# Kernel optimization log

Measured on AMD Instinct MI355X. Metric: run time of the kernel, lower is better.

The kernel has to match this reference:

```python
import jax, jax.numpy as jnp
import numpy as np

EMBED_DIM = 1024
FFN_DIM = 4096
N_QUBITS = 10


def setup_inputs() -> dict:
    key = jax.random.key(0)
    k_x, k_phi, k_w1, k_w2 = jax.random.split(key, 4)
    x = jax.random.normal(k_x, (8, 2048, EMBED_DIM), dtype=jnp.float32)
    # trainable RY angles, one per wire (torchquantum init ~ U(0, 2pi); any init works for a reference)
    ry_params = jax.random.uniform(k_phi, (N_QUBITS,), dtype=jnp.float32, minval=0.0, maxval=2.0 * np.pi)
    # nn.Linear(n_qubits, ffn_dim, bias=False): weight [ffn_dim, n_qubits]
    w1 = jax.random.normal(k_w1, (FFN_DIM, N_QUBITS), dtype=jnp.float32) / np.sqrt(N_QUBITS)
    # nn.Linear(ffn_dim, embed_dim, bias=False): weight [embed_dim, ffn_dim]
    w2 = jax.random.normal(k_w2, (EMBED_DIM, FFN_DIM), dtype=jnp.float32) / np.sqrt(FFN_DIM)
    return {"x": x, "ry_params": ry_params, "w1": w1, "w2": w2}


def reference(x, ry_params, w1, w2):
    # Quantum layer in closed form: wires are unentangled.
    # |0> --RX(x_i)--RY(phi_i)--> <Z_i> = cos(x_i) * cos(phi_i)
    # Only the first N_QUBITS features of each token are encoded.
    q_out = jnp.cos(x[..., :N_QUBITS]) * jnp.cos(ry_params)  # [B, S, nq]
    # dropout is identity in eval mode
    h = jnp.einsum('bsq,fq->bsf', q_out, w1)  # [B, S, ffn]
    h = jax.nn.relu(h)
    return jnp.einsum('bsf,ef->bse', h, w2)  # [B, S, embed]
```

## Files before the change

kernel.cpp:

```cpp
#include <hip/hip_runtime.h>
#include <stdint.h>

#define M_TOK   16384
#define EMBED   1024
#define FFN     4096
#define NQ      10

#define GK 4096
#define GN 1024
#define BK 64
#define NT (GK / BK)

typedef __attribute__((ext_vector_type(8))) short  bf16x8;
typedef __attribute__((ext_vector_type(4))) float  f32x4;
typedef __attribute__((ext_vector_type(8))) unsigned short u16x8;
typedef __attribute__((ext_vector_type(4))) unsigned short u16x4;

static __device__ __forceinline__ unsigned short f2bf(float f) {
    union { float f; unsigned u; } v; v.f = f;
    unsigned r = v.u + 0x7FFF + ((v.u >> 16) & 1);
    return (unsigned short)(r >> 16);
}

__global__ __launch_bounds__(256) void compute_h(
    const float* __restrict__ x, const float* __restrict__ ry,
    const float* __restrict__ w1, unsigned short* __restrict__ h)
{
    __shared__ float w1s[1024 * 11];
    __shared__ float cq[32 * 16];
    __shared__ float cry[16];

    const int tid = threadIdx.x;
    const int t0  = blockIdx.x * 32;
    const int f0  = blockIdx.y * 1024;

    if (tid < NQ) cry[tid] = cosf(ry[tid]);
    for (int idx = tid; idx < 32 * NQ; idx += 256) {
        int t = idx / NQ;
        int i = idx - t * NQ;
        cq[t * 16 + i] = cosf(x[(size_t)(t0 + t) * EMBED + i]);
    }
    for (int idx = tid; idx < (1024 * NQ) / 4; idx += 256) {
        float4 v = *(const float4*)(w1 + (size_t)f0 * NQ + idx * 4);
        int e = idx * 4;
#pragma unroll
        for (int k = 0; k < 4; ++k) {
            int ee = e + k;
            int r  = ee / NQ;
            int c  = ee - r * NQ;
            w1s[r * 11 + c] = ((const float*)&v)[k];
        }
    }
    __syncthreads();

    float wf[4][NQ];
#pragma unroll
    for (int fi = 0; fi < 4; ++fi)
#pragma unroll
        for (int i = 0; i < NQ; ++i)
            wf[fi][i] = w1s[(tid * 4 + fi) * 11 + i] * cry[i];

    for (int t = 0; t < 32; ++t) {
        const float4 c0 = *(const float4*)&cq[t * 16 + 0];
        const float4 c1 = *(const float4*)&cq[t * 16 + 4];
        const float2 c2 = *(const float2*)&cq[t * 16 + 8];
        u16x4 v;
#pragma unroll
        for (int fi = 0; fi < 4; ++fi) {
            float s = c0.x * wf[fi][0] + c0.y * wf[fi][1] + c0.z * wf[fi][2]
                    + c0.w * wf[fi][3] + c1.x * wf[fi][4] + c1.y * wf[fi][5]
                    + c1.z * wf[fi][6] + c1.w * wf[fi][7] + c2.x * wf[fi][8]
                    + c2.y * wf[fi][9];
            v[fi] = f2bf(fmaxf(s, 0.f));
        }
        *(u16x4*)(h + (size_t)(t0 + t) * FFN + f0 + tid * 4) = v;
    }
}

__global__ __launch_bounds__(256) void conv_w2(
    const float* __restrict__ w2, unsigned short* __restrict__ o)
{
    const int idx = (blockIdx.x * 256 + threadIdx.x) * 8;
    float4 a = *(const float4*)(w2 + idx);
    float4 b = *(const float4*)(w2 + idx + 4);
    u16x8 v;
    v[0] = f2bf(a.x); v[1] = f2bf(a.y); v[2] = f2bf(a.z); v[3] = f2bf(a.w);
    v[4] = f2bf(b.x); v[5] = f2bf(b.y); v[6] = f2bf(b.z); v[7] = f2bf(b.w);
    *(u16x8*)(o + idx) = v;
}

#define GL2LDS(g, l) \
    __builtin_amdgcn_global_load_lds( \
        (const __attribute__((address_space(1))) void*)(g), \
        (__attribute__((address_space(3))) void*)(l), 16, 0, 0)

__global__ __launch_bounds__(512, 2) void gemm_bt(
    const unsigned short* __restrict__ A,
    const unsigned short* __restrict__ B,
    float* __restrict__ C)
{
    __shared__ __align__(16) unsigned short As[2][256 * BK];
    __shared__ __align__(16) unsigned short Bs[2][256 * BK];

    const int tid  = threadIdx.x;
    const int wv   = tid >> 6;
    const int lane = tid & 63;
    const int wm   = wv >> 2;
    const int wn   = wv & 3;

    const int bid = blockIdx.x;
    const int wg  = (bid & 7) * 32 + (bid >> 3);
    const int m0  = (wg >> 2) * 256;
    const int n0  = (wg & 3) * 256;

    const int srow = lane >> 3;
    const int schk = (lane & 7) ^ srow;
    const char* ag = (const char*)A +
        ((size_t)(m0 + wv * 32 + srow) * GK + schk * 8) * 2;
    const char* bg = (const char*)B +
        ((size_t)(n0 + wv * 32 + srow) * GK + schk * 8) * 2;
    const int ldsb = (wv * 32) * 128;

    const int rr  = lane & 15;
    const int fsw = lane & 7;
    const int cc  = lane >> 4;

    f32x4 acc[8][4] = {};

#pragma unroll
    for (int l = 0; l < 4; ++l) {
        GL2LDS(ag + (size_t)l * 8 * (GK * 2), (char*)As[0] + ldsb + l * 1024);
        GL2LDS(bg + (size_t)l * 8 * (GK * 2), (char*)Bs[0] + ldsb + l * 1024);
    }
    asm volatile("s_waitcnt vmcnt(0)" ::: "memory");
    __builtin_amdgcn_s_barrier();

#pragma unroll 1
    for (int T = 0; T < NT; ++T) {
        const char* At = (const char*)As[T & 1];
        const char* Bt = (const char*)Bs[T & 1];

        if (T + 1 < NT) {
            char* Ad = (char*)As[(T + 1) & 1] + ldsb;
            char* Bd = (char*)Bs[(T + 1) & 1] + ldsb;
            const size_t ko = (size_t)(T + 1) * 128;
#pragma unroll
            for (int l = 0; l < 4; ++l) {
                GL2LDS(ag + ko + (size_t)l * 8 * (GK * 2), Ad + l * 1024);
                GL2LDS(bg + ko + (size_t)l * 8 * (GK * 2), Bd + l * 1024);
            }
        }

#pragma unroll
        for (int s = 0; s < 2; ++s) {
            const int choff = ((s * 4 + cc) ^ fsw) * 16;
            bf16x8 bfr[4], afr[4];
#pragma unroll
            for (int j = 0; j < 4; ++j)
                bfr[j] = *(const bf16x8*)(Bt + (wn * 64 + j * 16 + rr) * 128 + choff);
#pragma unroll
            for (int i = 0; i < 4; ++i)
                afr[i] = *(const bf16x8*)(At + (wm * 128 + i * 16 + rr) * 128 + choff);
            __builtin_amdgcn_s_setprio(1);
#pragma unroll
            for (int i = 0; i < 4; ++i)
#pragma unroll
                for (int j = 0; j < 4; ++j)
                    acc[i][j] = __builtin_amdgcn_mfma_f32_16x16x32_bf16(
                        afr[i], bfr[j], acc[i][j], 0, 0, 0);
            __builtin_amdgcn_s_setprio(0);
#pragma unroll
            for (int i = 0; i < 4; ++i)
                afr[i] = *(const bf16x8*)(At + (wm * 128 + 64 + i * 16 + rr) * 128 + choff);
            __builtin_amdgcn_s_setprio(1);
#pragma unroll
            for (int i = 0; i < 4; ++i)
#pragma unroll
                for (int j = 0; j < 4; ++j)
                    acc[4 + i][j] = __builtin_amdgcn_mfma_f32_16x16x32_bf16(
                        afr[i], bfr[j], acc[4 + i][j], 0, 0, 0);
            __builtin_amdgcn_s_setprio(0);
        }

        asm volatile("s_waitcnt vmcnt(0)" ::: "memory");
        __builtin_amdgcn_s_barrier();
    }

    const int cn = lane & 15;
    const int rb = (lane >> 4) * 4;
#pragma unroll
    for (int i = 0; i < 8; ++i)
#pragma unroll
        for (int j = 0; j < 4; ++j)
#pragma unroll
            for (int r = 0; r < 4; ++r) {
                const int m = m0 + wm * 128 + i * 16 + rb + r;
                const int n = n0 + wn * 64 + j * 16 + cn;
                C[(size_t)m * GN + n] = acc[i][j][r];
            }
}

extern "C" void kernel_launch(void* const* d_in, const int* in_sizes, int n_in,
                              void* d_out, int out_size, void* d_ws, size_t ws_size,
                              hipStream_t stream) {
    const float* x  = (const float*)d_in[0];
    const float* ry = (const float*)d_in[1];
    const float* w1 = (const float*)d_in[2];
    const float* w2 = (const float*)d_in[3];
    float* out = (float*)d_out;

    unsigned short* h   = (unsigned short*)d_ws;
    unsigned short* w2b = (unsigned short*)((char*)d_ws +
                           (size_t)M_TOK * FFN * sizeof(unsigned short));

    compute_h<<<dim3(512, 4), 256, 0, stream>>>(x, ry, w1, h);
    conv_w2<<<dim3((EMBED * FFN) / (256 * 8)), 256, 0, stream>>>(w2, w2b);
    gemm_bt<<<dim3(256), 512, 0, stream>>>(h, w2b, out);
}
```

Measured before the change: 284.3 us.

## Restructure GEMM main loop into quadrant phases interleaving staging with MFMA

The GEMM main loop now splits each K-tile into four quadrant phases (A-top/B-left, B-right, A-bottom), loading fragments for both K sub-steps up front. Global-to-LDS staging of the next tile is issued between phases, and barriers plus sched_barrier fences are placed around each phase. The aim is to overlap LDS reads and global prefetch with MFMA work, in the style of ping-pong scheduling across the two resident workgroups. Separately, compute_h drops the LDS copy of w1, reads w1 directly from global memory, and has each thread produce 8 features with 16-byte stores on a half-sized grid. The extra barriers add synchronisation overhead per tile.

Measured after the change: 266.3 us. -6.3%, faster.

```diff
diff --git a/kernel.cpp b/kernel.cpp
--- a/kernel.cpp
+++ b/kernel.cpp
@@ -14,7 +14,6 @@
 typedef __attribute__((ext_vector_type(8))) short  bf16x8;
 typedef __attribute__((ext_vector_type(4))) float  f32x4;
 typedef __attribute__((ext_vector_type(8))) unsigned short u16x8;
-typedef __attribute__((ext_vector_type(4))) unsigned short u16x4;
 
 static __device__ __forceinline__ unsigned short f2bf(float f) {
     union { float f; unsigned u; } v; v.f = f;
@@ -26,13 +25,12 @@
     const float* __restrict__ x, const float* __restrict__ ry,
     const float* __restrict__ w1, unsigned short* __restrict__ h)
 {
-    __shared__ float w1s[1024 * 11];
     __shared__ float cq[32 * 16];
-    __shared__ float cry[16];
+    __shared__ float cry[NQ];
 
     const int tid = threadIdx.x;
     const int t0  = blockIdx.x * 32;
-    const int f0  = blockIdx.y * 1024;
+    const int fb  = blockIdx.y * 2048 + tid * 8;
 
     if (tid < NQ) cry[tid] = cosf(ry[tid]);
     for (int idx = tid; idx < 32 * NQ; idx += 256) {
@@ -40,40 +38,29 @@
         int i = idx - t * NQ;
         cq[t * 16 + i] = cosf(x[(size_t)(t0 + t) * EMBED + i]);
     }
-    for (int idx = tid; idx < (1024 * NQ) / 4; idx += 256) {
-        float4 v = *(const float4*)(w1 + (size_t)f0 * NQ + idx * 4);
-        int e = idx * 4;
-#pragma unroll
-        for (int k = 0; k < 4; ++k) {
-            int ee = e + k;
-            int r  = ee / NQ;
-            int c  = ee - r * NQ;
-            w1s[r * 11 + c] = ((const float*)&v)[k];
-        }
-    }
     __syncthreads();
 
-    float wf[4][NQ];
-#pragma unroll
-    for (int fi = 0; fi < 4; ++fi)
+    float wf[8][NQ];
+#pragma unroll
+    for (int fi = 0; fi < 8; ++fi)
 #pragma unroll
         for (int i = 0; i < NQ; ++i)
-            wf[fi][i] = w1s[(tid * 4 + fi) * 11 + i] * cry[i];
+            wf[fi][i] = w1[(fb + fi) * NQ + i] * cry[i];
 
     for (int t = 0; t < 32; ++t) {
         const float4 c0 = *(const float4*)&cq[t * 16 + 0];
         const float4 c1 = *(const float4*)&cq[t * 16 + 4];
         const float2 c2 = *(const float2*)&cq[t * 16 + 8];
-        u16x4 v;
-#pragma unroll
-        for (int fi = 0; fi < 4; ++fi) {
+        u16x8 v;
+#pragma unroll
+        for (int fi = 0; fi < 8; ++fi) {
             float s = c0.x * wf[fi][0] + c0.y * wf[fi][1] + c0.z * wf[fi][2]
                     + c0.w * wf[fi][3] + c1.x * wf[fi][4] + c1.y * wf[fi][5]
                     + c1.z * wf[fi][6] + c1.w * wf[fi][7] + c2.x * wf[fi][8]
                     + c2.y * wf[fi][9];
             v[fi] = f2bf(fmaxf(s, 0.f));
         }
-        *(u16x4*)(h + (size_t)(t0 + t) * FFN + f0 + tid * 4) = v;
+        *(u16x8*)(h + (size_t)(t0 + t) * FFN + fb) = v;
     }
 }
 
@@ -113,25 +100,35 @@
     const int m0  = (wg >> 2) * 256;
     const int n0  = (wg & 3) * 256;
 
-    const int srow = lane >> 3;
-    const int schk = (lane & 7) ^ srow;
+    const int srow8 = lane >> 3;
+    const int schk  = (lane & 7) ^ srow8;
     const char* ag = (const char*)A +
-        ((size_t)(m0 + wv * 32 + srow) * GK + schk * 8) * 2;
+        ((size_t)(m0 + wv * 16 + srow8) * GK + schk * 8) * 2;
     const char* bg = (const char*)B +
-        ((size_t)(n0 + wv * 32 + srow) * GK + schk * 8) * 2;
-    const int ldsb = (wv * 32) * 128;
+        ((size_t)(n0 + wv * 16 + srow8) * GK + schk * 8) * 2;
+    const size_t ROW8 = (size_t)8 * GK * 2;
+    const size_t HALF = (size_t)128 * GK * 2;
+
+#define STAGE_A(buf, half, ko) do { \
+    GL2LDS(ag + (ko) + (half) * HALF,        (char*)As[buf] + ((half) * 128 + wv * 16) * 128); \
+    GL2LDS(ag + (ko) + (half) * HALF + ROW8, (char*)As[buf] + ((half) * 128 + wv * 16 + 8) * 128); \
+} while (0)
+#define STAGE_B(buf, half, ko) do { \
+    GL2LDS(bg + (ko) + (half) * HALF,        (char*)Bs[buf] + ((half) * 128 + wv * 16) * 128); \
+    GL2LDS(bg + (ko) + (half) * HALF + ROW8, (char*)Bs[buf] + ((half) * 128 + wv * 16 + 8) * 128); \
+} while (0)
 
     const int rr  = lane & 15;
     const int fsw = lane & 7;
     const int cc  = lane >> 4;
+#define CHOFF(s) ((((s) * 4 + cc) ^ fsw) * 16)
+#define AFRAG(mh, i, s) (*(const bf16x8*)(At + (wm * 128 + (mh) * 64 + (i) * 16 + rr) * 128 + CHOFF(s)))
+#define BFRAG(nh, j, s) (*(const bf16x8*)(Bt + (wn * 64 + (nh) * 32 + (j) * 16 + rr) * 128 + CHOFF(s)))
 
     f32x4 acc[8][4] = {};
 
-#pragma unroll
-    for (int l = 0; l < 4; ++l) {
-        GL2LDS(ag + (size_t)l * 8 * (GK * 2), (char*)As[0] + ldsb + l * 1024);
-        GL2LDS(bg + (size_t)l * 8 * (GK * 2), (char*)Bs[0] + ldsb + l * 1024);
-    }
+    STAGE_A(0, 0, 0); STAGE_A(0, 1, 0);
+    STAGE_B(0, 0, 0); STAGE_B(0, 1, 0);
     asm volatile("s_waitcnt vmcnt(0)" ::: "memory");
     __builtin_amdgcn_s_barrier();
 
@@ -139,49 +136,86 @@
     for (int T = 0; T < NT; ++T) {
         const char* At = (const char*)As[T & 1];
         const char* Bt = (const char*)Bs[T & 1];
-
-        if (T + 1 < NT) {
-            char* Ad = (char*)As[(T + 1) & 1] + ldsb;
-            char* Bd = (char*)Bs[(T + 1) & 1] + ldsb;
-            const size_t ko = (size_t)(T + 1) * 128;
-#pragma unroll
-            for (int l = 0; l < 4; ++l) {
-                GL2LDS(ag + ko + (size_t)l * 8 * (GK * 2), Ad + l * 1024);
-                GL2LDS(bg + ko + (size_t)l * 8 * (GK * 2), Bd + l * 1024);
-            }
+        const int nb   = (T + 1) & 1;
+        const size_t ko = (size_t)(T + 1) * 128;
+        const bool st  = (T + 1 < NT);
+
+        bf16x8 afr[2][4];
+        bf16x8 b0r[2][2];
+        bf16x8 b1r[2][2];
+
+#pragma unroll
+        for (int s = 0; s < 2; ++s) {
+#pragma unroll
+            for (int i = 0; i < 4; ++i) afr[s][i] = AFRAG(0, i, s);
+#pragma unroll
+            for (int j = 0; j < 2; ++j) b0r[s][j] = BFRAG(0, j, s);
         }
-
-#pragma unroll
-        for (int s = 0; s < 2; ++s) {
-            const int choff = ((s * 4 + cc) ^ fsw) * 16;
-            bf16x8 bfr[4], afr[4];
-#pragma unroll
-            for (int j = 0; j < 4; ++j)
-                bfr[j] = *(const bf16x8*)(Bt + (wn * 64 + j * 16 + rr) * 128 + choff);
-#pragma unroll
-            for (int i = 0; i < 4; ++i)
-                afr[i] = *(const bf16x8*)(At + (wm * 128 + i * 16 + rr) * 128 + choff);
-            __builtin_amdgcn_s_setprio(1);
-#pragma unroll
-            for (int i = 0; i < 4; ++i)
-#pragma unroll
-                for (int j = 0; j < 4; ++j)
+        if (st) { STAGE_A(nb, 0, ko); STAGE_A(nb, 1, ko); }
+        __builtin_amdgcn_s_barrier();
+        asm volatile("s_waitcnt lgkmcnt(0)" ::: "memory");
+        __builtin_amdgcn_sched_barrier(0);
+        __builtin_amdgcn_s_setprio(1);
+#pragma unroll
+        for (int s = 0; s < 2; ++s)
+#pragma unroll
+            for (int i = 0; i < 4; ++i)
+#pragma unroll
+                for (int j = 0; j < 2; ++j)
                     acc[i][j] = __builtin_amdgcn_mfma_f32_16x16x32_bf16(
-                        afr[i], bfr[j], acc[i][j], 0, 0, 0);
-            __builtin_amdgcn_s_setprio(0);
-#pragma unroll
-            for (int i = 0; i < 4; ++i)
-                afr[i] = *(const bf16x8*)(At + (wm * 128 + 64 + i * 16 + rr) * 128 + choff);
-            __builtin_amdgcn_s_setprio(1);
-#pragma unroll
-            for (int i = 0; i < 4; ++i)
-#pragma unroll
-                for (int j = 0; j < 4; ++j)
+                        afr[s][i], b0r[s][j], acc[i][j], 0, 0, 0);
+        __builtin_amdgcn_s_setprio(0);
+        __builtin_amdgcn_s_barrier();
+
+#pragma unroll
+        for (int s = 0; s < 2; ++s)
+#pragma unroll
+            for (int j = 0; j < 2; ++j) b1r[s][j] = BFRAG(1, j, s);
+        if (st) { STAGE_B(nb, 0, ko); STAGE_B(nb, 1, ko); }
+        __builtin_amdgcn_s_barrier();
+        asm volatile("s_waitcnt lgkmcnt(0)" ::: "memory");
+        __builtin_amdgcn_sched_barrier(0);
+        __builtin_amdgcn_s_setprio(1);
+#pragma unroll
+        for (int s = 0; s < 2; ++s)
+#pragma unroll
+            for (int i = 0; i < 4; ++i)
+#pragma unroll
+                for (int j = 0; j < 2; ++j)
+                    acc[i][2 + j] = __builtin_amdgcn_mfma_f32_16x16x32_bf16(
+                        afr[s][i], b1r[s][j], acc[i][2 + j], 0, 0, 0);
+        __builtin_amdgcn_s_setprio(0);
+        __builtin_amdgcn_s_barrier();
+
+#pragma unroll
+        for (int s = 0; s < 2; ++s)
+#pragma unroll
+            for (int i = 0; i < 4; ++i) afr[s][i] = AFRAG(1, i, s);
+        __builtin_amdgcn_s_barrier();
+        asm volatile("s_waitcnt lgkmcnt(0)" ::: "memory");
+        __builtin_amdgcn_sched_barrier(0);
+        __builtin_amdgcn_s_setprio(1);
+#pragma unroll
+        for (int s = 0; s < 2; ++s)
+#pragma unroll
+            for (int i = 0; i < 4; ++i)
+#pragma unroll
+                for (int j = 0; j < 2; ++j)
+                    acc[4 + i][2 + j] = __builtin_amdgcn_mfma_f32_16x16x32_bf16(
+                        afr[s][i], b1r[s][j], acc[4 + i][2 + j], 0, 0, 0);
+        __builtin_amdgcn_s_setprio(0);
+        __builtin_amdgcn_s_barrier();
+
+        __builtin_amdgcn_s_setprio(1);
+#pragma unroll
+        for (int s = 0; s < 2; ++s)
+#pragma unroll
+            for (int i = 0; i < 4; ++i)
+#pragma unroll
+                for (int j = 0; j < 2; ++j)
                     acc[4 + i][j] = __builtin_amdgcn_mfma_f32_16x16x32_bf16(
-                        afr[i], bfr[j], acc[4 + i][j], 0, 0, 0);
-            __builtin_amdgcn_s_setprio(0);
-        }
-
+                        afr[s][i], b0r[s][j], acc[4 + i][j], 0, 0, 0);
+        __builtin_amdgcn_s_setprio(0);
         asm volatile("s_waitcnt vmcnt(0)" ::: "memory");
         __builtin_amdgcn_s_barrier();
     }
@@ -213,7 +247,7 @@
     unsigned short* w2b = (unsigned short*)((char*)d_ws +
                            (size_t)M_TOK * FFN * sizeof(unsigned short));
 
-    compute_h<<<dim3(512, 4), 256, 0, stream>>>(x, ry, w1, h);
+    compute_h<<<dim3(512, 2), 256, 0, stream>>>(x, ry, w1, h);
     conv_w2<<<dim3((EMBED * FFN) / (256 * 8)), 256, 0, stream>>>(w2, w2b);
     gemm_bt<<<dim3(256), 512, 0, stream>>>(h, w2b, out);
 }
```
